# Kernel tuning notes

Measured on AMD Instinct MI355X. Metric: run time of the kernel, lower is better.

Reference implementation:

```python
import jax, jax.numpy as jnp
import numpy as np

D = 1024
F = 4096
EPS = 1e-5

def _layernorm(x, g, b):
    mu = jnp.mean(x, axis=-1, keepdims=True)
    var = jnp.mean(jnp.square(x - mu), axis=-1, keepdims=True)
    return (x - mu) * jax.lax.rsqrt(var + EPS) * g + b

def setup_inputs() -> dict:
    key = jax.random.key(0)
    ks = jax.random.split(key, 12)
    s = lambda fan_in: 1.0 / np.sqrt(fan_in)
    return {
        "x": jax.random.normal(ks[0], (4, 2048, D), dtype=jnp.float32),
        "ln1_g": jnp.ones((D,), jnp.float32),
        "ln1_b": jnp.zeros((D,), jnp.float32),
        "qkv_w": jax.random.uniform(ks[1], (D, 3 * D), jnp.float32, -s(D), s(D)),
        "qkv_b": jax.random.uniform(ks[2], (3 * D,), jnp.float32, -s(D), s(D)),
        "proj_w": jax.random.uniform(ks[3], (D, D), jnp.float32, -s(D), s(D)),
        "proj_b": jax.random.uniform(ks[4], (D,), jnp.float32, -s(D), s(D)),
        "ln2_g": jnp.ones((D,), jnp.float32),
        "ln2_b": jnp.zeros((D,), jnp.float32),
        "ff1_w": jax.random.uniform(ks[5], (D, F), jnp.float32, -s(D), s(D)),
        "ff1_b": jax.random.uniform(ks[6], (F,), jnp.float32, -s(D), s(D)),
        "ff2_w": jax.random.uniform(ks[7], (F, D), jnp.float32, -s(F), s(F)),
        "ff2_b": jax.random.uniform(ks[8], (D,), jnp.float32, -s(F), s(F)),
    }

def reference(x, ln1_g, ln1_b, qkv_w, qkv_b, proj_w, proj_b,
              ln2_g, ln2_b, ff1_w, ff1_b, ff2_w, ff2_b):
    B, T, C = x.shape
    h = _layernorm(x, ln1_g, ln1_b)
    qkv = h @ qkv_w + qkv_b                      # [B,T,3C]
    q, k, v = jnp.split(qkv, 3, axis=-1)
    att = jnp.einsum('btc,bsc->bts', q, k) / jnp.sqrt(jnp.float32(C))
    causal_mask = jnp.triu(jnp.ones((T, T), bool), 1)
    att = jnp.where(causal_mask, jnp.float32(-1e9), att)
    att = jax.nn.softmax(att, axis=-1)
    y = jnp.einsum('bts,bsc->btc', att, v)
    x = x + y @ proj_w + proj_b
    h2 = _layernorm(x, ln2_g, ln2_b)
    return x + jax.nn.relu(h2 @ ff1_w + ff1_b) @ ff2_w + ff2_b
```

## Files before the change

kernel.cpp:

```cpp
#include <hip/hip_runtime.h>
#include <hip/hip_bf16.h>

typedef __attribute__((ext_vector_type(8))) short bf16x8;
typedef __attribute__((ext_vector_type(4))) float f32x4;
using bf16 = __hip_bfloat16;

#define D_ 1024
#define T_ 2048
#define B_ 4
#define F_ 4096

__device__ __forceinline__ void gload_lds16(const void* g, void* l) {
  __builtin_amdgcn_global_load_lds(
      (const __attribute__((address_space(1))) void*)g,
      (__attribute__((address_space(3))) void*)l, 16, 0, 0);
}

__global__ __launch_bounds__(256) void ln_kernel(
    const float* __restrict__ x, const float* __restrict__ g,
    const float* __restrict__ b, bf16* __restrict__ out)
{
  int row = blockIdx.x;
  int tid = threadIdx.x;
  const float4 v = *reinterpret_cast<const float4*>(x + (size_t)row * D_ + tid * 4);
  float s = v.x + v.y + v.z + v.w;
  float q = v.x * v.x + v.y * v.y + v.z * v.z + v.w * v.w;
#pragma unroll
  for (int off = 32; off > 0; off >>= 1) {
    s += __shfl_down(s, off);
    q += __shfl_down(q, off);
  }
  __shared__ float psum[4], psq[4], stats[2];
  if ((tid & 63) == 0) { psum[tid >> 6] = s; psq[tid >> 6] = q; }
  __syncthreads();
  if (tid == 0) {
    float S = psum[0] + psum[1] + psum[2] + psum[3];
    float Q = psq[0] + psq[1] + psq[2] + psq[3];
    float mu = S * (1.0f / D_);
    float var = Q * (1.0f / D_) - mu * mu;
    stats[0] = mu;
    stats[1] = rsqrtf(var + 1e-5f);
  }
  __syncthreads();
  float mu = stats[0], rv = stats[1];
  const float4 gv = *reinterpret_cast<const float4*>(g + tid * 4);
  const float4 bv = *reinterpret_cast<const float4*>(b + tid * 4);
  bf16 o[4];
  o[0] = __float2bfloat16((v.x - mu) * rv * gv.x + bv.x);
  o[1] = __float2bfloat16((v.y - mu) * rv * gv.y + bv.y);
  o[2] = __float2bfloat16((v.z - mu) * rv * gv.z + bv.z);
  o[3] = __float2bfloat16((v.w - mu) * rv * gv.w + bv.w);
  *reinterpret_cast<ushort4*>(out + (size_t)row * D_ + tid * 4) =
      *reinterpret_cast<ushort4*>(o);
}

__global__ __launch_bounds__(256) void transpose_w_kernel(
    const float* __restrict__ in, bf16* __restrict__ out, int R, int C)
{
  __shared__ float t[32][33];
  int c0 = blockIdx.x * 32, r0 = blockIdx.y * 32;
  int c = threadIdx.x & 31, r8 = threadIdx.x >> 5;
#pragma unroll
  for (int i = 0; i < 4; ++i)
    t[r8 + i * 8][c] = in[(size_t)(r0 + r8 + i * 8) * C + c0 + c];
  __syncthreads();
#pragma unroll
  for (int i = 0; i < 4; ++i)
    out[(size_t)(c0 + r8 + i * 8) * R + r0 + c] = __float2bfloat16(t[c][r8 + i * 8]);
}

__global__ __launch_bounds__(256) void transpose_v_kernel(
    const bf16* __restrict__ qkv, bf16* __restrict__ vt)
{
  __shared__ bf16 t[32][34];
  int b = blockIdx.z;
  int c0 = blockIdx.x * 32;
  int r0 = blockIdx.y * 32;
  const bf16* in = qkv + (size_t)b * T_ * 3072 + 2 * D_;
  bf16* out = vt + (size_t)b * D_ * T_;
  int c = threadIdx.x & 31, r8 = threadIdx.x >> 5;
#pragma unroll
  for (int i = 0; i < 4; ++i)
    t[r8 + i * 8][c] = in[(size_t)(r0 + r8 + i * 8) * 3072 + c0 + c];
  __syncthreads();
#pragma unroll
  for (int i = 0; i < 4; ++i)
    out[(size_t)(c0 + r8 + i * 8) * T_ + r0 + c] = t[c][r8 + i * 8];
}

template <typename TOUT, bool RELU, bool TRI_SKIP, bool TRI_K>
__global__ __launch_bounds__(256) void gemm_bt_kernel(
    const bf16* __restrict__ A, int lda, long sAb,
    const bf16* __restrict__ Bt, int ldb, long sBb,
    const float* __restrict__ bias,
    const float* __restrict__ resid, int ldr, long sRb,
    TOUT* __restrict__ C, int ldc, long sCb,
    int K, float oscale)
{
  if (TRI_SKIP && blockIdx.x > blockIdx.y) return;
  __shared__ __align__(16) bf16 As[128 * 32];
  __shared__ __align__(16) bf16 Bs[128 * 32];
  const int tid = threadIdx.x;
  const int lane = tid & 63;
  const int w = __builtin_amdgcn_readfirstlane(tid >> 6);
  const int wm = w >> 1, wn = w & 1;
  const int m0 = blockIdx.y * 128, n0 = blockIdx.x * 128;
  const bf16* Ab = A + (size_t)blockIdx.z * sAb;
  const bf16* Bb = Bt + (size_t)blockIdx.z * sBb;

  const int srow = lane >> 2;
  const int sko = (lane & 3) * 8;
  const int kmax = TRI_K ? (blockIdx.y + 1) * 128 : K;

  f32x4 acc[4][4] = {};
  for (int kt = 0; kt < kmax; kt += 32) {
    __syncthreads();
#pragma unroll
    for (int i = 0; i < 2; ++i) {
      int c = w * 2 + i;
      gload_lds16(Ab + (size_t)(m0 + c * 16 + srow) * lda + kt + sko, &As[c * 512]);
      gload_lds16(Bb + (size_t)(n0 + c * 16 + srow) * ldb + kt + sko, &Bs[c * 512]);
    }
    __syncthreads();
    const int koff = (lane >> 4) * 8;
    bf16x8 aF[4], bF[4];
#pragma unroll
    for (int m = 0; m < 4; ++m)
      aF[m] = *reinterpret_cast<const bf16x8*>(&As[(wm * 64 + m * 16 + (lane & 15)) * 32 + koff]);
#pragma unroll
    for (int n = 0; n < 4; ++n)
      bF[n] = *reinterpret_cast<const bf16x8*>(&Bs[(wn * 64 + n * 16 + (lane & 15)) * 32 + koff]);
#pragma unroll
    for (int m = 0; m < 4; ++m)
#pragma unroll
      for (int n = 0; n < 4; ++n)
        acc[m][n] = __builtin_amdgcn_mfma_f32_16x16x32_bf16(aF[m], bF[n], acc[m][n], 0, 0, 0);
  }

  const float* Rb = resid ? resid + (size_t)blockIdx.z * sRb : nullptr;
  TOUT* Cb = C + (size_t)blockIdx.z * sCb;
#pragma unroll
  for (int n = 0; n < 4; ++n) {
    int gc = n0 + wn * 64 + n * 16 + (lane & 15);
    float bv = bias ? bias[gc] : 0.0f;
#pragma unroll
    for (int m = 0; m < 4; ++m) {
      int gr = m0 + wm * 64 + m * 16 + ((lane >> 4) << 2);
#pragma unroll
      for (int j = 0; j < 4; ++j) {
        float v = acc[m][n][j] * oscale + bv;
        if (RELU) v = fmaxf(v, 0.0f);
        int row = gr + j;
        if (Rb) v += Rb[(size_t)row * ldr + gc];
        if constexpr (sizeof(TOUT) == 2)
          Cb[(size_t)row * ldc + gc] = __float2bfloat16(v);
        else
          Cb[(size_t)row * ldc + gc] = v;
      }
    }
  }
}

__global__ __launch_bounds__(256) void softmax_kernel(float* __restrict__ S)
{
  const int w = threadIdx.x >> 6, lane = threadIdx.x & 63;
  const int t = blockIdx.x * 4 + w;
  const int b = blockIdx.z;
  float* Srow = S + ((size_t)b * T_ + t) * T_;
  const int Keff = ((t >> 7) + 1) << 7;

  float4 vals[8];
  float mx = -1e30f;
#pragma unroll
  for (int c = 0; c < 8; ++c) {
    int col = c * 256 + lane * 4;
    if (col < Keff) {
      vals[c] = *reinterpret_cast<const float4*>(Srow + col);
#pragma unroll
      for (int j = 0; j < 4; ++j)
        if (col + j <= t) mx = fmaxf(mx, ((float*)&vals[c])[j]);
    } else {
      vals[c] = float4{0.f, 0.f, 0.f, 0.f};
    }
  }
#pragma unroll
  for (int off = 32; off > 0; off >>= 1) mx = fmaxf(mx, __shfl_xor(mx, off));

  float sum = 0.f;
#pragma unroll
  for (int c = 0; c < 8; ++c) {
    int col = c * 256 + lane * 4;
#pragma unroll
    for (int j = 0; j < 4; ++j) {
      float e = (col + j <= t) ? __expf(((float*)&vals[c])[j] - mx) : 0.f;
      ((float*)&vals[c])[j] = e;
      sum += e;
    }
  }
#pragma unroll
  for (int off = 32; off > 0; off >>= 1) sum += __shfl_xor(sum, off);
  const float inv = 1.0f / sum;

  bf16* Prow = (bf16*)Srow;
#pragma unroll
  for (int c = 0; c < 8; ++c) {
    int col = c * 256 + lane * 4;
    if (col < Keff) {
      bf16 o[4];
#pragma unroll
      for (int j = 0; j < 4; ++j) o[j] = __float2bfloat16(((float*)&vals[c])[j] * inv);
      *reinterpret_cast<ushort4*>(Prow + col) = *reinterpret_cast<ushort4*>(o);
    }
  }
}

extern "C" void kernel_launch(void* const* d_in, const int* in_sizes, int n_in,
                              void* d_out, int out_size, void* d_ws, size_t ws_size,
                              hipStream_t stream)
{
  const float* x      = (const float*)d_in[0];
  const float* ln1_g  = (const float*)d_in[1];
  const float* ln1_b  = (const float*)d_in[2];
  const float* qkv_w  = (const float*)d_in[3];
  const float* qkv_b  = (const float*)d_in[4];
  const float* proj_w = (const float*)d_in[5];
  const float* proj_b = (const float*)d_in[6];
  const float* ln2_g  = (const float*)d_in[7];
  const float* ln2_b  = (const float*)d_in[8];
  const float* ff1_w  = (const float*)d_in[9];
  const float* ff1_b  = (const float*)d_in[10];
  const float* ff2_w  = (const float*)d_in[11];
  const float* ff2_b  = (const float*)d_in[12];
  float* out = (float*)d_out;

  char* ws = (char*)d_ws;
  bf16*  qkvb    = (bf16*)(ws);
  bf16*  y       = (bf16*)(ws);
  bf16*  proj_wT = (bf16*)(ws + 16777216L);
  bf16*  ff1_wT  = (bf16*)(ws + 18874368L);
  bf16*  ff2_wT  = (bf16*)(ws + 27262976L);
  bf16*  h2      = (bf16*)(ws + 35651584L);
  bf16*  h       = (bf16*)(ws + 50331648L);
  bf16*  VT      = (bf16*)(ws + 50331648L);
  bf16*  qkv_wT  = (bf16*)(ws + 67108864L);
  float* Sbuf    = (float*)(ws + 67108864L);
  bf16*  Pbuf    = (bf16*)(ws + 67108864L);
  bf16*  ff1o    = (bf16*)(ws + 67108864L);

  const int R = B_ * T_;

  transpose_w_kernel<<<dim3(3072 / 32, 1024 / 32), 256, 0, stream>>>(qkv_w, qkv_wT, 1024, 3072);
  ln_kernel<<<dim3(R), 256, 0, stream>>>(x, ln1_g, ln1_b, h);
  gemm_bt_kernel<bf16, false, false, false><<<dim3(3072 / 128, R / 128, 1), 256, 0, stream>>>(
      h, D_, 0, qkv_wT, D_, 0, qkv_b, nullptr, 0, 0, qkvb, 3072, 0, D_, 1.0f);
  transpose_v_kernel<<<dim3(D_ / 32, T_ / 32, B_), 256, 0, stream>>>(qkvb, VT);
  gemm_bt_kernel<float, false, true, false><<<dim3(T_ / 128, T_ / 128, B_), 256, 0, stream>>>(
      qkvb, 3072, (long)T_ * 3072, qkvb + D_, 3072, (long)T_ * 3072,
      nullptr, nullptr, 0, 0, Sbuf, T_, (long)T_ * T_, D_, 0.03125f);
  softmax_kernel<<<dim3(T_ / 4, 1, B_), 256, 0, stream>>>(Sbuf);
  transpose_w_kernel<<<dim3(1024 / 32, 1024 / 32), 256, 0, stream>>>(proj_w, proj_wT, 1024, 1024);
  transpose_w_kernel<<<dim3(4096 / 32, 1024 / 32), 256, 0, stream>>>(ff1_w, ff1_wT, 1024, 4096);
  transpose_w_kernel<<<dim3(1024 / 32, 4096 / 32), 256, 0, stream>>>(ff2_w, ff2_wT, 4096, 1024);
  gemm_bt_kernel<bf16, false, false, true><<<dim3(D_ / 128, T_ / 128, B_), 256, 0, stream>>>(
      Pbuf, 4096, (long)T_ * 4096, VT, T_, (long)D_ * T_,
      nullptr, nullptr, 0, 0, y, D_, (long)T_ * D_, T_, 1.0f);
  gemm_bt_kernel<float, false, false, false><<<dim3(D_ / 128, R / 128, 1), 256, 0, stream>>>(
      y, D_, 0, proj_wT, D_, 0, proj_b, x, D_, 0, out, D_, 0, D_, 1.0f);
  ln_kernel<<<dim3(R), 256, 0, stream>>>(out, ln2_g, ln2_b, h2);
  gemm_bt_kernel<bf16, true, false, false><<<dim3(F_ / 128, R / 128, 1), 256, 0, stream>>>(
      h2, D_, 0, ff1_wT, D_, 0, ff1_b, nullptr, 0, 0, ff1o, F_, 0, D_, 1.0f);
  gemm_bt_kernel<float, false, false, false><<<dim3(D_ / 128, R / 128, 1), 256, 0, stream>>>(
      ff1o, F_, 0, ff2_wT, F_, 0, ff2_b, out, D_, 0, out, D_, 0, F_, 1.0f);
}
```

Before: 629.3 us.

## Add 256-row tiled double-buffered GEMM kernel for dense projection GEMMs

Introduces a 512-thread GEMM kernel with 256xBN tiles (BN 256 or 128), a K-step of 64, XOR-swizzled LDS, and two-stage global-to-LDS prefetch synchronised with explicit vmcnt waits. It replaces the 128x128 GEMM for the QKV, output projection, FF1 and FF2 matmuls. The aim is more operand reuse per LDS load and better overlap of global loads with MFMA work. The cost is much larger LDS use and many more accumulator registers, which can lower occupancy, and the hand-set vmcnt counts have to match the number of loads issued per stage.

Result: faster. 597.3 us (-5.1%).

```diff
diff --git a/kernel.cpp b/kernel.cpp
--- a/kernel.cpp
+++ b/kernel.cpp
@@ -86,6 +86,134 @@
 #pragma unroll
   for (int i = 0; i < 4; ++i)
     out[(size_t)(c0 + r8 + i * 8) * T_ + r0 + c] = t[c][r8 + i * 8];
+}
+
+template <int NFRAG, typename TOUT, bool RELU>
+__global__ __launch_bounds__(512) void gemm256_kernel(
+    const bf16* __restrict__ A, int lda,
+    const bf16* __restrict__ Bt, int ldb,
+    const float* __restrict__ bias,
+    const float* __restrict__ resid, int ldr,
+    TOUT* __restrict__ C, int ldc,
+    int K)
+{
+  constexpr int BN = 64 * NFRAG;
+  constexpr int BBYTES = BN * 128;
+  constexpr int BCHW = BN / 64;
+  __shared__ __align__(16) char lds[2 * (32768 + BBYTES)];
+
+  const int tid = threadIdx.x;
+  const int lane = tid & 63;
+  const int w = __builtin_amdgcn_readfirstlane(tid >> 6);
+  const int wm = w >> 2;
+  const int wn = w & 3;
+  const int m0 = blockIdx.y * 256, n0 = blockIdx.x * BN;
+
+  const int srow8 = lane >> 3;
+  const int skb = ((lane & 7) ^ srow8) * 16;
+
+  const char* Ag = (const char*)A;
+  const char* Bg = (const char*)Bt;
+  const long ldab = (long)lda * 2, ldbb = (long)ldb * 2;
+  const int nt = K >> 6;
+
+  auto stage = [&](int bi, int t) {
+    char* base = lds + bi * (32768 + BBYTES);
+    long kt2 = (long)t * 128;
+#pragma unroll
+    for (int i = 0; i < 4; ++i) {
+      int c = w * 4 + i;
+      gload_lds16(Ag + (size_t)(m0 + c * 8 + srow8) * ldab + kt2 + skb,
+                  base + c * 1024);
+    }
+#pragma unroll
+    for (int i = 0; i < BCHW; ++i) {
+      int c = w * BCHW + i;
+      gload_lds16(Bg + (size_t)(n0 + c * 8 + srow8) * ldbb + kt2 + skb,
+                  base + 32768 + c * 1024);
+    }
+  };
+
+  stage(0, 0);
+  stage(1, 1);
+
+  f32x4 acc[8][NFRAG] = {};
+
+  for (int t = 0; t < nt; ++t) {
+    if (t < nt - 1) {
+      if constexpr (NFRAG == 4) asm volatile("s_waitcnt vmcnt(8)" ::: "memory");
+      else                      asm volatile("s_waitcnt vmcnt(6)" ::: "memory");
+    } else {
+      asm volatile("s_waitcnt vmcnt(0)" ::: "memory");
+    }
+    __builtin_amdgcn_s_barrier();
+    asm volatile("" ::: "memory");
+
+    const char* Ab = lds + (t & 1) * (32768 + BBYTES);
+    const char* Bb = Ab + 32768;
+    const int l15 = lane & 15;
+    const int kbb = (lane >> 4) * 16;
+
+#pragma unroll
+    for (int mh = 0; mh < 2; ++mh) {
+      bf16x8 aF[4][2];
+#pragma unroll
+      for (int mi = 0; mi < 4; ++mi)
+#pragma unroll
+        for (int ks = 0; ks < 2; ++ks) {
+          int row = wm * 128 + mh * 64 + mi * 16 + l15;
+          int kb = ks * 64 + kbb;
+          aF[mi][ks] = *reinterpret_cast<const bf16x8*>(
+              Ab + row * 128 + (kb ^ ((row & 7) << 4)));
+        }
+#pragma unroll
+      for (int nh = 0; nh < (NFRAG / 2); ++nh) {
+        bf16x8 bF[2][2];
+#pragma unroll
+        for (int ni = 0; ni < 2; ++ni)
+#pragma unroll
+          for (int ks = 0; ks < 2; ++ks) {
+            int row = wn * (NFRAG * 16) + nh * 32 + ni * 16 + l15;
+            int kb = ks * 64 + kbb;
+            bF[ni][ks] = *reinterpret_cast<const bf16x8*>(
+                Bb + row * 128 + (kb ^ ((row & 7) << 4)));
+          }
+        __builtin_amdgcn_s_setprio(1);
+#pragma unroll
+        for (int mi = 0; mi < 4; ++mi)
+#pragma unroll
+          for (int ni = 0; ni < 2; ++ni)
+#pragma unroll
+            for (int ks = 0; ks < 2; ++ks)
+              acc[mh * 4 + mi][nh * 2 + ni] = __builtin_amdgcn_mfma_f32_16x16x32_bf16(
+                  aF[mi][ks], bF[ni][ks], acc[mh * 4 + mi][nh * 2 + ni], 0, 0, 0);
+        __builtin_amdgcn_s_setprio(0);
+      }
+    }
+    __builtin_amdgcn_s_barrier();
+    asm volatile("" ::: "memory");
+    if (t + 2 < nt) stage(t & 1, t + 2);
+  }
+
+#pragma unroll
+  for (int nf = 0; nf < NFRAG; ++nf) {
+    int gc = n0 + wn * (NFRAG * 16) + nf * 16 + (lane & 15);
+    float bv = bias ? bias[gc] : 0.0f;
+#pragma unroll
+    for (int mf = 0; mf < 8; ++mf) {
+      int gr = m0 + wm * 128 + mf * 16 + ((lane >> 4) << 2);
+#pragma unroll
+      for (int j = 0; j < 4; ++j) {
+        float v = acc[mf][nf][j] + bv;
+        if (RELU) v = fmaxf(v, 0.0f);
+        if (resid) v += resid[(size_t)(gr + j) * ldr + gc];
+        if constexpr (sizeof(TOUT) == 2)
+          C[(size_t)(gr + j) * ldc + gc] = __float2bfloat16(v);
+        else
+          C[(size_t)(gr + j) * ldc + gc] = v;
+      }
+    }
+  }
 }
 
 template <typename TOUT, bool RELU, bool TRI_SKIP, bool TRI_K>
@@ -251,8 +379,8 @@
 
   transpose_w_kernel<<<dim3(3072 / 32, 1024 / 32), 256, 0, stream>>>(qkv_w, qkv_wT, 1024, 3072);
   ln_kernel<<<dim3(R), 256, 0, stream>>>(x, ln1_g, ln1_b, h);
-  gemm_bt_kernel<bf16, false, false, false><<<dim3(3072 / 128, R / 128, 1), 256, 0, stream>>>(
-      h, D_, 0, qkv_wT, D_, 0, qkv_b, nullptr, 0, 0, qkvb, 3072, 0, D_, 1.0f);
+  gemm256_kernel<4, bf16, false><<<dim3(3072 / 256, R / 256), 512, 0, stream>>>(
+      h, D_, qkv_wT, D_, qkv_b, nullptr, 0, qkvb, 3072, D_);
   transpose_v_kernel<<<dim3(D_ / 32, T_ / 32, B_), 256, 0, stream>>>(qkvb, VT);
   gemm_bt_kernel<float, false, true, false><<<dim3(T_ / 128, T_ / 128, B_), 256, 0, stream>>>(
       qkvb, 3072, (long)T_ * 3072, qkvb + D_, 3072, (long)T_ * 3072,
@@ -264,11 +392,11 @@
   gemm_bt_kernel<bf16, false, false, true><<<dim3(D_ / 128, T_ / 128, B_), 256, 0, stream>>>(
       Pbuf, 4096, (long)T_ * 4096, VT, T_, (long)D_ * T_,
       nullptr, nullptr, 0, 0, y, D_, (long)T_ * D_, T_, 1.0f);
-  gemm_bt_kernel<float, false, false, false><<<dim3(D_ / 128, R / 128, 1), 256, 0, stream>>>(
-      y, D_, 0, proj_wT, D_, 0, proj_b, x, D_, 0, out, D_, 0, D_, 1.0f);
+  gemm256_kernel<2, float, false><<<dim3(D_ / 128, R / 256), 512, 0, stream>>>(
+      y, D_, proj_wT, D_, proj_b, x, D_, out, D_, D_);
   ln_kernel<<<dim3(R), 256, 0, stream>>>(out, ln2_g, ln2_b, h2);
-  gemm_bt_kernel<bf16, true, false, false><<<dim3(F_ / 128, R / 128, 1), 256, 0, stream>>>(
-      h2, D_, 0, ff1_wT, D_, 0, ff1_b, nullptr, 0, 0, ff1o, F_, 0, D_, 1.0f);
-  gemm_bt_kernel<float, false, false, false><<<dim3(D_ / 128, R / 128, 1), 256, 0, stream>>>(
-      ff1o, F_, 0, ff2_wT, F_, 0, ff2_b, out, D_, 0, out, D_, 0, F_, 1.0f);
-}
+  gemm256_kernel<4, bf16, true><<<dim3(F_ / 256, R / 256), 512, 0, stream>>>(
+      h2, D_, ff1_wT, D_, ff1_b, nullptr, 0, ff1o, F_, D_);
+  gemm256_kernel<2, float, false><<<dim3(D_ / 128, R / 256), 512, 0, stream>>>(
+      ff1o, F_, ff2_wT, F_, ff2_b, out, D_, out, D_, F_);
+}
```

## Add 8-wave ping-pong GEMM with larger tiles for dense projections

Applied to the files above, without the earlier changes.

Adds a new 512-thread GEMM kernel with 256-row tiles, double-buffered LDS staging via direct global-to-LDS loads, XOR-swizzled LDS layout, and a barrier-interleaved schedule that splits each K tile into four MFMA quadrants with priority boosts. The kernel also remaps workgroups to group neighbouring tiles for better L2 reuse. It replaces the older 128x128 GEMM for the QKV, output projection, FF1 and FF2 matmuls, with 64-row-per-wave tiles used for the N=1024 outputs. The goal is to overlap global loads with MFMA work and raise data reuse per tile. The cost is heavy LDS use and many barriers, which may limit occupancy or stall waves.

Result: faster. 555.8 us (-11.7%).

```diff
diff --git a/kernel.cpp b/kernel.cpp
--- a/kernel.cpp
+++ b/kernel.cpp
@@ -86,6 +86,193 @@
 #pragma unroll
   for (int i = 0; i < 4; ++i)
     out[(size_t)(c0 + r8 + i * 8) * T_ + r0 + c] = t[c][r8 + i * 8];
+}
+
+#define BAR_() do { asm volatile("" ::: "memory"); __builtin_amdgcn_s_barrier(); \
+                    asm volatile("" ::: "memory"); } while (0)
+#define LGKM0_() asm volatile("s_waitcnt lgkmcnt(0)" ::: "memory")
+
+template <int WM, typename TOUT, bool RELU>
+__global__ __launch_bounds__(512) void gemm8p_kernel(
+    const bf16* __restrict__ A, int lda,
+    const bf16* __restrict__ Bt, int ldb,
+    const float* __restrict__ bias,
+    const float* __restrict__ resid, int ldr,
+    TOUT* __restrict__ C, int ldc, int K)
+{
+  constexpr int NW = (WM == 128) ? 4 : 2;
+  constexpr int BN = NW * 64;
+  constexpr int MF = WM / 16;
+  constexpr int MQF = MF / 2;
+  constexpr int ABUF = 32768;
+  constexpr int BBUF = BN * 128;
+  constexpr int BUFSZ = ABUF + BBUF;
+  constexpr int BCW = BN / 128;
+  __shared__ __align__(16) char lds[2 * BUFSZ];
+
+  const int tid = threadIdx.x;
+  const int lane = tid & 63;
+  const int w = __builtin_amdgcn_readfirstlane(tid >> 6);
+  const int wm = (WM == 128) ? (w >> 2) : (w >> 1);
+  const int wn = (WM == 128) ? (w & 3) : (w & 1);
+
+  const int nwg = gridDim.x * gridDim.y;
+  const int flat = blockIdx.y * gridDim.x + blockIdx.x;
+  const int sw = (flat & 7) * (nwg >> 3) + (flat >> 3);
+  const int m0 = (sw / gridDim.x) * 256;
+  const int n0 = (sw % gridDim.x) * BN;
+
+  const int srow8 = lane >> 3;
+  const int skb = ((lane & 7) ^ srow8) * 16;
+  const char* Ag = (const char*)A;
+  const char* Bg = (const char*)Bt;
+  const long ldab = (long)lda * 2, ldbb = (long)ldb * 2;
+  const int nt = K >> 6;
+
+  char* buf0 = lds;
+  char* buf1 = lds + BUFSZ;
+
+#define STAGE_A(buf, t, half)                                                     \
+  do {                                                                            \
+    _Pragma("unroll")                                                             \
+    for (int i_ = 0; i_ < 2; ++i_) {                                              \
+      int c_ = w * 2 + i_;                                                        \
+      gload_lds16(Ag + (size_t)(m0 + (half)*128 + c_ * 8 + srow8) * ldab +        \
+                      (long)(t)*128 + skb,                                        \
+                  (buf) + (half)*16384 + c_ * 1024);                              \
+    }                                                                             \
+  } while (0)
+
+#define STAGE_B(buf, t, half)                                                     \
+  do {                                                                            \
+    _Pragma("unroll")                                                             \
+    for (int i_ = 0; i_ < BCW; ++i_) {                                            \
+      int c_ = w * BCW + i_;                                                      \
+      gload_lds16(Bg + (size_t)(n0 + (half) * (BN / 2) + c_ * 8 + srow8) * ldbb + \
+                      (long)(t)*128 + skb,                                        \
+                  (buf) + ABUF + (half) * (BBUF / 2) + c_ * 1024);                \
+    }                                                                             \
+  } while (0)
+
+  const int l15 = lane & 15;
+  const int kb16 = (lane >> 4) * 16;
+  const int aHalf = (wm * WM) / 128;
+  const int aBase = (wm * WM) % 128;
+  const int bHalf = (wn * 64) / (BN / 2);
+  const int bBase = (wn * 64) % (BN / 2);
+
+#define READ_A(dst, buf, mq)                                                      \
+  do {                                                                            \
+    _Pragma("unroll")                                                             \
+    for (int mi_ = 0; mi_ < MQF; ++mi_) {                                         \
+      _Pragma("unroll")                                                           \
+      for (int ks_ = 0; ks_ < 2; ++ks_) {                                         \
+        int row_ = aBase + ((mq)*MQF + mi_) * 16 + l15;                           \
+        dst[mi_][ks_] = *reinterpret_cast<const bf16x8*>(                         \
+            (buf) + aHalf * 16384 + row_ * 128 +                                  \
+            ((ks_ * 64 + kb16) ^ ((row_ & 7) << 4)));                             \
+      }                                                                           \
+    }                                                                             \
+  } while (0)
+
+#define READ_B(dst, buf, nq)                                                      \
+  do {                                                                            \
+    _Pragma("unroll")                                                             \
+    for (int ni_ = 0; ni_ < 2; ++ni_) {                                           \
+      _Pragma("unroll")                                                           \
+      for (int ks_ = 0; ks_ < 2; ++ks_) {                                         \
+        int row_ = bBase + ((nq)*2 + ni_) * 16 + l15;                             \
+        dst[ni_][ks_] = *reinterpret_cast<const bf16x8*>(                         \
+            (buf) + ABUF + bHalf * (BBUF / 2) + row_ * 128 +                      \
+            ((ks_ * 64 + kb16) ^ ((row_ & 7) << 4)));                             \
+      }                                                                           \
+    }                                                                             \
+  } while (0)
+
+#define MFMA_Q(af, bf, mq, nq)                                                    \
+  do {                                                                            \
+    __builtin_amdgcn_s_setprio(1);                                                \
+    _Pragma("unroll")                                                             \
+    for (int mi_ = 0; mi_ < MQF; ++mi_) {                                         \
+      _Pragma("unroll")                                                           \
+      for (int ni_ = 0; ni_ < 2; ++ni_) {                                         \
+        _Pragma("unroll")                                                         \
+        for (int ks_ = 0; ks_ < 2; ++ks_)                                         \
+          acc[(mq)*MQF + mi_][(nq)*2 + ni_] =                                     \
+              __builtin_amdgcn_mfma_f32_16x16x32_bf16(                            \
+                  af[mi_][ks_], bf[ni_][ks_],                                     \
+                  acc[(mq)*MQF + mi_][(nq)*2 + ni_], 0, 0, 0);                    \
+      }                                                                           \
+    }                                                                             \
+    __builtin_amdgcn_s_setprio(0);                                                \
+  } while (0)
+
+#define VM_CNT()                                                                  \
+  do {                                                                            \
+    if constexpr (WM == 128) asm volatile("s_waitcnt vmcnt(6)" ::: "memory");     \
+    else                     asm volatile("s_waitcnt vmcnt(4)" ::: "memory");     \
+  } while (0)
+
+  f32x4 acc[MF][4] = {};
+  bf16x8 aF0[MQF][2], aF1[MQF][2], bF0[2][2], bF1[2][2];
+
+  STAGE_B(buf0, 0, 0); STAGE_B(buf0, 0, 1); STAGE_A(buf0, 0, 0); STAGE_A(buf0, 0, 1);
+  STAGE_B(buf1, 1, 0); STAGE_B(buf1, 1, 1); STAGE_A(buf1, 1, 0);
+  VM_CNT();
+  BAR_();
+
+  for (int t0 = 0; t0 < nt; t0 += 2) {
+    const int t1 = t0 + 1, t2 = t0 + 2, t3 = t0 + 3;
+    const bool more = (t2 < nt);
+    READ_A(aF0, buf0, 0); READ_B(bF0, buf0, 0);
+    STAGE_A(buf1, t1, 1);
+    BAR_(); LGKM0_(); MFMA_Q(aF0, bF0, 0, 0); BAR_();
+    READ_B(bF1, buf0, 1);
+    BAR_(); LGKM0_(); MFMA_Q(aF0, bF1, 0, 1); BAR_();
+    READ_A(aF1, buf0, 1);
+    if (more) { STAGE_B(buf0, t2, 0); STAGE_B(buf0, t2, 1); }
+    BAR_(); LGKM0_(); MFMA_Q(aF1, bF1, 1, 1); BAR_();
+    if (more) { STAGE_A(buf0, t2, 0); VM_CNT(); }
+    else      { asm volatile("s_waitcnt vmcnt(0)" ::: "memory"); }
+    BAR_(); MFMA_Q(aF1, bF0, 1, 0); BAR_();
+    READ_A(aF0, buf1, 0); READ_B(bF0, buf1, 0);
+    if (more) STAGE_A(buf0, t2, 1);
+    BAR_(); LGKM0_(); MFMA_Q(aF0, bF0, 0, 0); BAR_();
+    READ_B(bF1, buf1, 1);
+    BAR_(); LGKM0_(); MFMA_Q(aF0, bF1, 0, 1); BAR_();
+    READ_A(aF1, buf1, 1);
+    if (more) { STAGE_B(buf1, t3, 0); STAGE_B(buf1, t3, 1); }
+    BAR_(); LGKM0_(); MFMA_Q(aF1, bF1, 1, 1); BAR_();
+    if (more) { STAGE_A(buf1, t3, 0); VM_CNT(); }
+    else      { asm volatile("s_waitcnt vmcnt(0)" ::: "memory"); }
+    BAR_(); MFMA_Q(aF1, bF0, 1, 0); BAR_();
+  }
+
+#pragma unroll
+  for (int nf = 0; nf < 4; ++nf) {
+    int gc = n0 + wn * 64 + nf * 16 + l15;
+    float bv = bias ? bias[gc] : 0.0f;
+#pragma unroll
+    for (int mf = 0; mf < MF; ++mf) {
+      int gr = m0 + wm * WM + mf * 16 + ((lane >> 4) << 2);
+#pragma unroll
+      for (int j = 0; j < 4; ++j) {
+        float v = acc[mf][nf][j] + bv;
+        if (RELU) v = fmaxf(v, 0.0f);
+        if (resid) v += resid[(size_t)(gr + j) * ldr + gc];
+        if constexpr (sizeof(TOUT) == 2)
+          C[(size_t)(gr + j) * ldc + gc] = __float2bfloat16(v);
+        else
+          C[(size_t)(gr + j) * ldc + gc] = v;
+      }
+    }
+  }
+#undef STAGE_A
+#undef STAGE_B
+#undef READ_A
+#undef READ_B
+#undef MFMA_Q
+#undef VM_CNT
 }
 
 template <typename TOUT, bool RELU, bool TRI_SKIP, bool TRI_K>
@@ -251,8 +438,8 @@
 
   transpose_w_kernel<<<dim3(3072 / 32, 1024 / 32), 256, 0, stream>>>(qkv_w, qkv_wT, 1024, 3072);
   ln_kernel<<<dim3(R), 256, 0, stream>>>(x, ln1_g, ln1_b, h);
-  gemm_bt_kernel<bf16, false, false, false><<<dim3(3072 / 128, R / 128, 1), 256, 0, stream>>>(
-      h, D_, 0, qkv_wT, D_, 0, qkv_b, nullptr, 0, 0, qkvb, 3072, 0, D_, 1.0f);
+  gemm8p_kernel<128, bf16, false><<<dim3(3072 / 256, R / 256), 512, 0, stream>>>(
+      h, D_, qkv_wT, D_, qkv_b, nullptr, 0, qkvb, 3072, D_);
   transpose_v_kernel<<<dim3(D_ / 32, T_ / 32, B_), 256, 0, stream>>>(qkvb, VT);
   gemm_bt_kernel<float, false, true, false><<<dim3(T_ / 128, T_ / 128, B_), 256, 0, stream>>>(
       qkvb, 3072, (long)T_ * 3072, qkvb + D_, 3072, (long)T_ * 3072,
@@ -264,11 +451,11 @@
   gemm_bt_kernel<bf16, false, false, true><<<dim3(D_ / 128, T_ / 128, B_), 256, 0, stream>>>(
       Pbuf, 4096, (long)T_ * 4096, VT, T_, (long)D_ * T_,
       nullptr, nullptr, 0, 0, y, D_, (long)T_ * D_, T_, 1.0f);
-  gemm_bt_kernel<float, false, false, false><<<dim3(D_ / 128, R / 128, 1), 256, 0, stream>>>(
-      y, D_, 0, proj_wT, D_, 0, proj_b, x, D_, 0, out, D_, 0, D_, 1.0f);
+  gemm8p_kernel<64, float, false><<<dim3(D_ / 128, R / 256), 512, 0, stream>>>(
+      y, D_, proj_wT, D_, proj_b, x, D_, out, D_, D_);
   ln_kernel<<<dim3(R), 256, 0, stream>>>(out, ln2_g, ln2_b, h2);
-  gemm_bt_kernel<bf16, true, false, false><<<dim3(F_ / 128, R / 128, 1), 256, 0, stream>>>(
-      h2, D_, 0, ff1_wT, D_, 0, ff1_b, nullptr, 0, 0, ff1o, F_, 0, D_, 1.0f);
-  gemm_bt_kernel<float, false, false, false><<<dim3(D_ / 128, R / 128, 1), 256, 0, stream>>>(
-      ff1o, F_, 0, ff2_wT, F_, 0, ff2_b, out, D_, 0, out, D_, 0, F_, 1.0f);
-}
+  gemm8p_kernel<128, bf16, true><<<dim3(F_ / 256, R / 256), 512, 0, stream>>>(
+      h2, D_, ff1_wT, D_, ff1_b, nullptr, 0, ff1o, F_, D_);
+  gemm8p_kernel<64, float, false><<<dim3(D_ / 128, R / 256), 512, 0, stream>>>(
+      ff1o, F_, ff2_wT, F_, ff2_b, out, D_, out, D_, F_);
+}
```
